# Optimization experiments

Measured on AMD Instinct MI355X. Metric: run time of the kernel, lower is better.

The kernel has to match this reference:

```python
import jax, jax.numpy as jnp
import numpy as np

B, C, H, W = 8, 192, 128, 128
HEADS = 16
EPS = 1e-12  # F.normalize eps


def setup_inputs() -> dict:
    key = jax.random.key(0)
    k1, k2, k3, k4 = jax.random.split(key, 4)
    s = 0.02
    return {
        "x": jax.random.normal(k1, (B, C, H, W), dtype=jnp.float32),
        "w_qkv": jax.random.normal(k2, (3 * C, C), dtype=jnp.float32) * s,
        "w_dw": jax.random.normal(k3, (C, 1, 3, 3), dtype=jnp.float32) * s,
        "w_proj": jax.random.normal(k4, (C, C), dtype=jnp.float32) * s,
        "temperature": jnp.ones((HEADS, 1, 1), dtype=jnp.float32),
    }


def reference(x, w_qkv, w_dw, w_proj, temperature):
    b, c, h, w = x.shape
    heads = HEADS
    hd = c // heads  # per-head channel dim
    hw = h * w

    # 1x1 conv qkv projection: [b, 3c, h, w]
    qkv = jnp.einsum('bchw,oc->bohw', x, w_qkv)
    q, k, v = jnp.split(qkv, 3, axis=1)

    def to_heads(t):
        return t.reshape(b, heads, hd, hw)  # b head c (h w)

    q, k, v = to_heads(q), to_heads(k), to_heads(v)

    # L2-normalize along spatial dim (matches F.normalize with eps clamp)
    q = q / jnp.maximum(jnp.linalg.norm(q, axis=-1, keepdims=True), EPS)
    k = k / jnp.maximum(jnp.linalg.norm(k, axis=-1, keepdims=True), EPS)

    # channel-wise attention: [b, head, hd, hd]
    attn = jnp.einsum('bhcn,bhdn->bhcd', q, k) * temperature
    attn = jax.nn.softmax(attn, axis=-1)

    out = jnp.einsum('bhcd,bhdn->bhcn', attn, v)  # [b, head, hd, hw]
    out = out.reshape(b, c, h, w)

    # depthwise 3x3 conv, padding=1
    out = jax.lax.conv_general_dilated(
        out, w_dw, window_strides=(1, 1), padding=((1, 1), (1, 1)),
        dimension_numbers=('NCHW', 'OIHW', 'NCHW'), feature_group_count=c)

    # 1x1 conv projection
    out = jnp.einsum('bchw,oc->bohw', out, w_proj)
    return out
```

## Files before the change

### kernel.cpp

```cpp
#include <hip/hip_runtime.h>

#define B_   8
#define C_   192
#define HW_  16384
#define W_   128
#define NH_  16
#define HD_  12

#define OFF_G      0u
#define OFF_WQKV   1179648u
#define OFF_WDW    1622016u
#define OFF_TEMP   1628928u
#define OFF_WPROJ  1629184u
#define OFF_M      1702912u
#define OFF_Y      2292736u

typedef __attribute__((ext_vector_type(8))) __bf16 bf16x8;
typedef __attribute__((ext_vector_type(8))) short  short8;
typedef __attribute__((ext_vector_type(4))) short  short4v;
typedef __attribute__((ext_vector_type(4))) float  floatx4;

__device__ __forceinline__ unsigned short f2bfu(float f) {
  union { float f; unsigned u; } v; v.f = f;
  unsigned r = (v.u + 0x7FFFu + ((v.u >> 16) & 1u)) >> 16;
  return (unsigned short)r;
}
__device__ __forceinline__ float bfu2f(unsigned short h) {
  union { unsigned u; float f; } v; v.u = ((unsigned)h) << 16;
  return v.f;
}
__device__ __forceinline__ bool bfmode(const void* temp) {
  return ((const unsigned*)temp)[0] != 0x3F800000u;
}
__device__ __forceinline__ float in_ld(const void* p, int i, bool bf) {
  return bf ? bfu2f(((const unsigned short*)p)[i]) : ((const float*)p)[i];
}
__device__ __forceinline__ floatx4 mfma16(short8 a, short8 b, floatx4 c) {
  union U { short8 s; bf16x8 b; } ua, ub;
  ua.s = a; ub.s = b;
  return __builtin_amdgcn_mfma_f32_16x16x32_bf16(ua.b, ub.b, c, 0, 0, 0);
}
__device__ __forceinline__ short8 row_frag(const void* x, bool bf, long elemoff) {
  short8 r;
  if (bf) {
    r = *(const short8*)((const unsigned short*)x + elemoff);
  } else {
    const float4* p4 = (const float4*)((const float*)x + elemoff);
    float4 a = p4[0], b = p4[1];
    r[0] = (short)f2bfu(a.x); r[1] = (short)f2bfu(a.y);
    r[2] = (short)f2bfu(a.z); r[3] = (short)f2bfu(a.w);
    r[4] = (short)f2bfu(b.x); r[5] = (short)f2bfu(b.y);
    r[6] = (short)f2bfu(b.z); r[7] = (short)f2bfu(b.w);
  }
  return r;
}

__global__ __launch_bounds__(256) void k_init(const void* wqkv, const void* wdw,
                                              const void* wproj, const void* temp,
                                              unsigned char* ws) {
  bool bf = bfmode(temp);
  int i = blockIdx.x * 256 + threadIdx.x;
  if (i < 110592) { ((float*)(ws + OFF_WQKV))[i] = in_ld(wqkv, i, bf); return; }
  i -= 110592;
  if (i < 1728) { ((float*)(ws + OFF_WDW))[i] = in_ld(wdw, i, bf); return; }
  i -= 1728;
  if (i < 16) { ((float*)(ws + OFF_TEMP))[i] = in_ld(temp, i, bf); return; }
  i -= 16;
  if (i < 36864) {
    unsigned short* wp = (unsigned short*)(ws + OFF_WPROJ);
    wp[i] = bf ? ((const unsigned short*)wproj)[i] : f2bfu(((const float*)wproj)[i]);
  }
}

__global__ __launch_bounds__(512) void k_gram(const void* x, const void* temp,
                                              unsigned char* ws) {
  bool bf = bfmode(temp);
  float* GP = (float*)(ws + OFF_Y);
  int b = blockIdx.x >> 5, grp = blockIdx.x & 31;
  int tid = threadIdx.x;
  int w = tid >> 6, lane = tid & 63, m = lane & 15, q = lane >> 4;
  int r0 = (w >> 1) * 3, c0 = (w & 1) * 6;
  long xb = (long)b * C_ * HW_;
  __shared__ __align__(16) short xs[C_][136];
  floatx4 acc[3][6];
  floatx4 zz = {0.f, 0.f, 0.f, 0.f};
#pragma unroll
  for (int i = 0; i < 3; ++i)
#pragma unroll
    for (int t = 0; t < 6; ++t) acc[i][t] = zz;

  short8 st[6];
  {
    int px0 = grp * 512;
#pragma unroll
    for (int i = 0; i < 6; ++i) {
      int chunk = i * 512 + tid;
      int c = chunk >> 4, p8 = chunk & 15;
      st[i] = row_frag(x, bf, xb + (long)c * HW_ + px0 + p8 * 8);
    }
  }
  for (int sl = 0; sl < 4; ++sl) {
    if (sl) __syncthreads();
#pragma unroll
    for (int i = 0; i < 6; ++i) {
      int chunk = i * 512 + tid;
      int c = chunk >> 4, p8 = chunk & 15;
      *(short8*)&xs[c][p8 * 8] = st[i];
    }
    __syncthreads();
    if (sl < 3) {
      int px0 = grp * 512 + (sl + 1) * 128;
#pragma unroll
      for (int i = 0; i < 6; ++i) {
        int chunk = i * 512 + tid;
        int c = chunk >> 4, p8 = chunk & 15;
        st[i] = row_frag(x, bf, xb + (long)c * HW_ + px0 + p8 * 8);
      }
    }
#pragma unroll
    for (int ks = 0; ks < 4; ++ks) {
      int col = ks * 32 + q * 8;
      short8 A0 = *(const short8*)&xs[(r0 + 0) * 16 + m][col];
      short8 A1 = *(const short8*)&xs[(r0 + 1) * 16 + m][col];
      short8 A2 = *(const short8*)&xs[(r0 + 2) * 16 + m][col];
#pragma unroll
      for (int t = 0; t < 6; ++t) {
        short8 F = *(const short8*)&xs[(c0 + t) * 16 + m][col];
        acc[0][t] = mfma16(A0, F, acc[0][t]);
        acc[1][t] = mfma16(A1, F, acc[1][t]);
        acc[2][t] = mfma16(A2, F, acc[2][t]);
      }
    }
  }
  float* GPb = GP + (long)(b * 32 + grp) * (C_ * C_);
#pragma unroll
  for (int i = 0; i < 3; ++i)
#pragma unroll
    for (int t = 0; t < 6; ++t)
#pragma unroll
      for (int r = 0; r < 4; ++r)
        GPb[((r0 + i) * 16 + q * 4 + r) * C_ + (c0 + t) * 16 + m] = acc[i][t][r];
}

__global__ __launch_bounds__(256) void k_reduce(unsigned char* ws) {
  const float4* GP = (const float4*)(ws + OFF_Y);
  float4* G = (float4*)(ws + OFF_G);
  int idx = blockIdx.x * 256 + threadIdx.x;
  int b = idx / 9216;
  int i = idx - b * 9216;
  const float4* p = GP + (long)b * 32 * 9216 + i;
  float4 s = {0.f, 0.f, 0.f, 0.f};
#pragma unroll
  for (int g = 0; g < 32; ++g) {
    float4 v = p[(long)g * 9216];
    s.x += v.x; s.y += v.y; s.z += v.z; s.w += v.w;
  }
  G[(long)b * 9216 + i] = s;
}

__global__ __launch_bounds__(256) void k_attn(unsigned char* ws) {
  int b = blockIdx.x >> 4, h = blockIdx.x & 15;
  int tid = threadIdx.x;
  const float* G  = (const float*)(ws + OFF_G) + (long)b * C_ * C_;
  const float* Wf = (const float*)(ws + OFF_WQKV);
  const float* Wq = Wf + (h * HD_) * C_;
  const float* Wk = Wf + (C_ + h * HD_) * C_;
  const float* Wv = Wf + (2 * C_ + h * HD_) * C_;
  float tmprt = ((const float*)(ws + OFF_TEMP))[h];
  unsigned short* Mh = (unsigned short*)(ws + OFF_M) + ((long)b * C_ + h * HD_) * C_;

  __shared__ float Gs[32][C_ + 1];
  __shared__ float tq[HD_][C_], tk[HD_][C_];
  __shared__ float Sm[HD_][HD_], Aw[HD_][HD_], nq[HD_], nk[HD_];

  for (int jblk = 0; jblk < 6; ++jblk) {
    for (int i = tid; i < 32 * C_; i += 256) {
      int jj = i / C_, a = i - jj * C_;
      Gs[jj][a] = G[(jblk * 32 + jj) * C_ + a];
    }
    __syncthreads();
    for (int i = tid; i < 2 * HD_ * 32; i += 256) {
      int jj = i & 31, rest = i >> 5;
      int c = rest % HD_, which = rest / HD_;
      const float* Wrow = (which ? Wk : Wq) + c * C_;
      float s = 0.f;
      for (int a = 0; a < C_; ++a) s += Wrow[a] * Gs[jj][a];
      float (*dst)[C_] = which ? tk : tq;
      dst[c][jblk * 32 + jj] = s;
    }
    __syncthreads();
  }
  if (tid < 144) {
    int c = tid / HD_, d = tid - c * HD_;
    float s = 0.f;
    for (int a = 0; a < C_; ++a) s += tq[c][a] * Wk[d * C_ + a];
    Sm[c][d] = s;
  } else if (tid < 156) {
    int c = tid - 144; float s = 0.f;
    for (int a = 0; a < C_; ++a) s += tq[c][a] * Wq[c * C_ + a];
    nq[c] = s;
  } else if (tid < 168) {
    int c = tid - 156; float s = 0.f;
    for (int a = 0; a < C_; ++a) s += tk[c][a] * Wk[c * C_ + a];
    nk[c] = s;
  }
  __syncthreads();
  if (tid < HD_) {
    int c = tid;
    float qn = fmaxf(sqrtf(fmaxf(nq[c], 0.f)), 1e-12f);
    float L[HD_], mx = -1e30f;
    for (int d = 0; d < HD_; ++d) {
      float kn = fmaxf(sqrtf(fmaxf(nk[d], 0.f)), 1e-12f);
      L[d] = Sm[c][d] / (qn * kn) * tmprt;
      mx = fmaxf(mx, L[d]);
    }
    float ssum = 0.f;
    for (int d = 0; d < HD_; ++d) { L[d] = __expf(L[d] - mx); ssum += L[d]; }
    float inv = 1.f / ssum;
    for (int d = 0; d < HD_; ++d) Aw[c][d] = L[d] * inv;
  }
  __syncthreads();
  for (int i = tid; i < HD_ * C_; i += 256) {
    int c = i / C_, j = i - c * C_;
    float s = 0.f;
    for (int d = 0; d < HD_; ++d) s += Aw[c][d] * Wv[d * C_ + j];
    Mh[c * C_ + j] = f2bfu(s);
  }
}

__global__ __launch_bounds__(256) void k_mx(const void* x, const void* temp,
                                            unsigned char* ws) {
  bool bf = bfmode(temp);
  const unsigned short* Mb = (const unsigned short*)(ws + OFF_M);
  unsigned short* y = (unsigned short*)(ws + OFF_Y);
  int b = blockIdx.x >> 7, px0 = (blockIdx.x & 127) * 128;
  int tid = threadIdx.x;
  int w = tid >> 6, lane = tid & 63, m = lane & 15, q = lane >> 4;
  long xb = (long)b * C_ * HW_;
  __shared__ __align__(16) short xsT[128][200];
  for (int i = 0; i < 3; ++i) {
    int chunk = i * 256 + tid;
    int p8 = chunk & 15, cq = chunk >> 4;
    short8 r0 = row_frag(x, bf, xb + (long)(cq * 4 + 0) * HW_ + px0 + p8 * 8);
    short8 r1 = row_frag(x, bf, xb + (long)(cq * 4 + 1) * HW_ + px0 + p8 * 8);
    short8 r2 = row_frag(x, bf, xb + (long)(cq * 4 + 2) * HW_ + px0 + p8 * 8);
    short8 r3 = row_frag(x, bf, xb + (long)(cq * 4 + 3) * HW_ + px0 + p8 * 8);
    for (int j = 0; j < 8; ++j) {
      short4v v = { r0[j], r1[j], r2[j], r3[j] };
      *(short4v*)&xsT[p8 * 8 + j][cq * 4] = v;
    }
  }
  __syncthreads();
  floatx4 acc[3][8];
  floatx4 zz = {0.f, 0.f, 0.f, 0.f};
  for (int i = 0; i < 3; ++i)
    for (int pt = 0; pt < 8; ++pt) acc[i][pt] = zz;
  for (int k = 0; k < 6; ++k) {
    int c0 = k * 32;
    const unsigned short* Mrow = Mb + (long)b * C_ * C_ + c0 + q * 8;
    short8 A0 = *(const short8*)(Mrow + ((3 * w + 0) * 16 + m) * C_);
    short8 A1 = *(const short8*)(Mrow + ((3 * w + 1) * 16 + m) * C_);
    short8 A2 = *(const short8*)(Mrow + ((3 * w + 2) * 16 + m) * C_);
    for (int pt = 0; pt < 8; ++pt) {
      short8 Bf = *(const short8*)&xsT[pt * 16 + m][c0 + q * 8];
      acc[0][pt] = mfma16(A0, Bf, acc[0][pt]);
      acc[1][pt] = mfma16(A1, Bf, acc[1][pt]);
      acc[2][pt] = mfma16(A2, Bf, acc[2][pt]);
    }
  }
  for (int i = 0; i < 3; ++i) {
    int rowb = (3 * w + i) * 16 + q * 4;
    for (int pt = 0; pt < 8; ++pt) {
      int px = px0 + pt * 16 + m;
      for (int rg = 0; rg < 4; ++rg)
        y[((long)b * C_ + rowb + rg) * HW_ + px] = f2bfu(acc[i][pt][rg]);
    }
  }
}

__global__ __launch_bounds__(512) void k_out(const void* temp, unsigned char* ws,
                                             void* out) {
  bool bf = bfmode(temp);
  const unsigned short* y = (const unsigned short*)(ws + OFF_Y);
  const float* wdw = (const float*)(ws + OFF_WDW);
  const unsigned short* Wp = (const unsigned short*)(ws + OFF_WPROJ);
  int b = blockIdx.x >> 7, irow = blockIdx.x & 127;
  int tid = threadIdx.x;
  __shared__ __align__(16) unsigned dly[128 * 36];

  int wv = tid >> 6, lane = tid & 63, m = lane & 15, q = lane >> 4;
  int wr = wv >> 2, wc = wv & 3;
  int pA = wc * 32 + m, pB = pA + 16;
  int swzA = (pA >> 3) & 7, swzB = (pB >> 3) & 7;

  int oct = tid & 15, cg = tid >> 4;
  int p0 = oct * 8;
  int wbase = p0 * 36 + ((((cg >> 2) ^ (oct & 7)) << 2) | (cg & 3));

  floatx4 acc[6][2];
  floatx4 zz = {0.f, 0.f, 0.f, 0.f};
#pragma unroll
  for (int r = 0; r < 6; ++r) { acc[r][0] = zz; acc[r][1] = zz; }

  for (int ch = 0; ch < 3; ++ch) {
    if (ch) __syncthreads();
    float a0[8], a1[8];
#pragma unroll
    for (int i = 0; i < 8; ++i) { a0[i] = 0.f; a1[i] = 0.f; }
#pragma unroll
    for (int j = 0; j < 2; ++j) {
      float* aj = j ? a1 : a0;
      int c = ch * 64 + cg * 2 + j;
      const unsigned short* yc = y + ((long)b * C_ + c) * HW_;
      float wv9[9];
#pragma unroll
      for (int t = 0; t < 9; ++t) wv9[t] = wdw[c * 9 + t];
      for (int dy = 0; dy < 3; ++dy) {
        int rr = irow + dy - 1;
        if (rr < 0 || rr > 127) continue;
        const unsigned short* yr = yc + rr * W_;
        float v[10];
        v[0] = (p0 == 0) ? 0.f : bfu2f(yr[p0 - 1]);
        union { uint4 u; unsigned short s[8]; } uu;
        uu.u = *(const uint4*)(yr + p0);
#pragma unroll
        for (int i = 0; i < 8; ++i) v[1 + i] = bfu2f(uu.s[i]);
        v[9] = (p0 + 8 >= W_) ? 0.f : bfu2f(yr[p0 + 8]);
#pragma unroll
        for (int dx = 0; dx < 3; ++dx) {
          float wc9 = wv9[dy * 3 + dx];
#pragma unroll
          for (int i = 0; i < 8; ++i) aj[i] += wc9 * v[i + dx];
        }
      }
    }
#pragma unroll
    for (int i = 0; i < 8; ++i) {
      unsigned pk = (unsigned)f2bfu(a0[i]) | ((unsigned)f2bfu(a1[i]) << 16);
      dly[wbase + i * 36] = pk;
    }
    __syncthreads();
#pragma unroll
    for (int ks = 0; ks < 2; ++ks) {
      int kb = ks * 4 + q;
      short8 B0 = *(const short8*)&dly[pA * 36 + ((kb ^ swzA) << 2)];
      short8 B1 = *(const short8*)&dly[pB * 36 + ((kb ^ swzB) << 2)];
      int c0 = ch * 64 + ks * 32 + q * 8;
#pragma unroll
      for (int r = 0; r < 6; ++r) {
        short8 A = *(const short8*)(Wp + (wr * 96 + r * 16 + m) * C_ + c0);
        acc[r][0] = mfma16(A, B0, acc[r][0]);
        acc[r][1] = mfma16(A, B1, acc[r][1]);
      }
    }
  }
  long ob = (long)b * C_ * HW_ + irow * W_;
#pragma unroll
  for (int r = 0; r < 6; ++r) {
    int o = wr * 96 + r * 16 + q * 4;
#pragma unroll
    for (int rg = 0; rg < 4; ++rg) {
      long off = ob + (long)(o + rg) * HW_;
      float v0 = acc[r][0][rg], v1 = acc[r][1][rg];
      if (bf) {
        ((unsigned short*)out)[off + pA] = f2bfu(v0);
        ((unsigned short*)out)[off + pB] = f2bfu(v1);
      } else {
        ((float*)out)[off + pA] = v0;
        ((float*)out)[off + pB] = v1;
      }
    }
  }
}

extern "C" void kernel_launch(void* const* d_in, const int* in_sizes, int n_in,
                              void* d_out, int out_size, void* d_ws, size_t ws_size,
                              hipStream_t stream) {
  const void* x     = d_in[0];
  const void* wqkv  = d_in[1];
  const void* wdw   = d_in[2];
  const void* wproj = d_in[3];
  const void* temp  = d_in[4];
  unsigned char* ws = (unsigned char*)d_ws;
  k_init<<<dim3(583), dim3(256), 0, stream>>>(wqkv, wdw, wproj, temp, ws);
  k_gram<<<dim3(256), dim3(512), 0, stream>>>(x, temp, ws);
  k_reduce<<<dim3(288), dim3(256), 0, stream>>>(ws);
  k_attn<<<dim3(128), dim3(256), 0, stream>>>(ws);
  k_mx<<<dim3(1024), dim3(256), 0, stream>>>(x, temp, ws);
  k_out<<<dim3(1024), dim3(512), 0, stream>>>(temp, ws, d_out);
}
```

Baseline: 349.1 us.

## Software-pipeline depthwise conv loads in k_out with register double buffering

Restructures the k_out kernel so the global loads for the next 64-channel chunk are issued into a second register buffer while the current chunk's depthwise conv and MFMA projection run. Horizontal halo values now come from wave shuffles instead of extra scalar global loads. Depthwise weights are staged once in shared memory. The block index is remapped to interleave batches across consecutive blocks. The aim is to hide global memory latency and cut redundant loads, at the cost of more registers (two 6×uint4 buffers), which may reduce occupancy.

```diff
diff --git a/kernel.cpp b/kernel.cpp
--- a/kernel.cpp
+++ b/kernel.cpp
@@ -284,9 +284,11 @@
   const unsigned short* y = (const unsigned short*)(ws + OFF_Y);
   const float* wdw = (const float*)(ws + OFF_WDW);
   const unsigned short* Wp = (const unsigned short*)(ws + OFF_WPROJ);
-  int b = blockIdx.x >> 7, irow = blockIdx.x & 127;
+  int lg = (blockIdx.x & 7) * 128 + (blockIdx.x >> 3);
+  int b = lg >> 7, irow = lg & 127;
   int tid = threadIdx.x;
   __shared__ __align__(16) unsigned dly[128 * 36];
+  __shared__ float dwlds[C_ * 9];
 
   int wv = tid >> 6, lane = tid & 63, m = lane & 15, q = lane >> 4;
   int wr = wv >> 2, wc = wv & 3;
@@ -297,63 +299,106 @@
   int p0 = oct * 8;
   int wbase = p0 * 36 + ((((cg >> 2) ^ (oct & 7)) << 2) | (cg & 3));
 
+  bool v_lo = irow > 0, v_hi = irow < 127;
+  int rlo = (v_lo ? irow - 1 : 0) * W_;
+  int rmi = irow * W_;
+  int rhi = (v_hi ? irow + 1 : 127) * W_;
+  const unsigned short* ybase = y + (long)b * C_ * HW_;
+
   floatx4 acc[6][2];
   floatx4 zz = {0.f, 0.f, 0.f, 0.f};
 #pragma unroll
   for (int r = 0; r < 6; ++r) { acc[r][0] = zz; acc[r][1] = zz; }
 
-  for (int ch = 0; ch < 3; ++ch) {
-    if (ch) __syncthreads();
-    float a0[8], a1[8];
-#pragma unroll
-    for (int i = 0; i < 8; ++i) { a0[i] = 0.f; a1[i] = 0.f; }
-#pragma unroll
-    for (int j = 0; j < 2; ++j) {
-      float* aj = j ? a1 : a0;
-      int c = ch * 64 + cg * 2 + j;
-      const unsigned short* yc = y + ((long)b * C_ + c) * HW_;
-      float wv9[9];
-#pragma unroll
-      for (int t = 0; t < 9; ++t) wv9[t] = wdw[c * 9 + t];
-      for (int dy = 0; dy < 3; ++dy) {
-        int rr = irow + dy - 1;
-        if (rr < 0 || rr > 127) continue;
-        const unsigned short* yr = yc + rr * W_;
-        float v[10];
-        v[0] = (p0 == 0) ? 0.f : bfu2f(yr[p0 - 1]);
-        union { uint4 u; unsigned short s[8]; } uu;
-        uu.u = *(const uint4*)(yr + p0);
-#pragma unroll
-        for (int i = 0; i < 8; ++i) v[1 + i] = bfu2f(uu.s[i]);
-        v[9] = (p0 + 8 >= W_) ? 0.f : bfu2f(yr[p0 + 8]);
-#pragma unroll
-        for (int dx = 0; dx < 3; ++dx) {
-          float wc9 = wv9[dy * 3 + dx];
-#pragma unroll
-          for (int i = 0; i < 8; ++i) aj[i] += wc9 * v[i + dx];
-        }
-      }
-    }
-#pragma unroll
-    for (int i = 0; i < 8; ++i) {
-      unsigned pk = (unsigned)f2bfu(a0[i]) | ((unsigned)f2bfu(a1[i]) << 16);
-      dly[wbase + i * 36] = pk;
-    }
-    __syncthreads();
-#pragma unroll
-    for (int ks = 0; ks < 2; ++ks) {
-      int kb = ks * 4 + q;
-      short8 B0 = *(const short8*)&dly[pA * 36 + ((kb ^ swzA) << 2)];
-      short8 B1 = *(const short8*)&dly[pB * 36 + ((kb ^ swzB) << 2)];
-      int c0 = ch * 64 + ks * 32 + q * 8;
-#pragma unroll
-      for (int r = 0; r < 6; ++r) {
-        short8 A = *(const short8*)(Wp + (wr * 96 + r * 16 + m) * C_ + c0);
-        acc[r][0] = mfma16(A, B0, acc[r][0]);
-        acc[r][1] = mfma16(A, B1, acc[r][1]);
-      }
-    }
-  }
+#define ISSUE(CH, L) { \
+  const unsigned short* yc0 = ybase + (long)((CH) * 64 + cg * 2) * HW_; \
+  const unsigned short* yc1 = yc0 + HW_; \
+  (L)[0] = *(const uint4*)(yc0 + rlo + p0); \
+  (L)[1] = *(const uint4*)(yc0 + rmi + p0); \
+  (L)[2] = *(const uint4*)(yc0 + rhi + p0); \
+  (L)[3] = *(const uint4*)(yc1 + rlo + p0); \
+  (L)[4] = *(const uint4*)(yc1 + rmi + p0); \
+  (L)[5] = *(const uint4*)(yc1 + rhi + p0); \
+}
+
+#define DWHALF(Lp, AJ, CC) { \
+  float w9[9]; \
+  _Pragma("unroll") \
+  for (int t = 0; t < 9; ++t) w9[t] = dwlds[(CC) * 9 + t]; \
+  _Pragma("unroll") \
+  for (int dy = 0; dy < 3; ++dy) { \
+    bool valid = (dy == 1) || (dy == 0 ? v_lo : v_hi); \
+    uint4 uu = (Lp)[dy]; \
+    unsigned lw = (unsigned)__shfl_up((int)uu.w, 1); \
+    unsigned rw = (unsigned)__shfl_down((int)uu.x, 1); \
+    if (valid) { \
+      union { uint4 u; unsigned short s[8]; } cv; cv.u = uu; \
+      float v[10]; \
+      v[0] = (oct == 0) ? 0.f : bfu2f((unsigned short)(lw >> 16)); \
+      _Pragma("unroll") \
+      for (int i = 0; i < 8; ++i) v[1 + i] = bfu2f(cv.s[i]); \
+      v[9] = (oct == 15) ? 0.f : bfu2f((unsigned short)(rw & 0xffffu)); \
+      _Pragma("unroll") \
+      for (int dx = 0; dx < 3; ++dx) { \
+        float wc9 = w9[dy * 3 + dx]; \
+        _Pragma("unroll") \
+        for (int i = 0; i < 8; ++i) (AJ)[i] += wc9 * v[i + dx]; \
+      } \
+    } \
+  } }
+
+#define DWCOMP(L, CH) { \
+  float a0[8], a1[8]; \
+  _Pragma("unroll") \
+  for (int i = 0; i < 8; ++i) { a0[i] = 0.f; a1[i] = 0.f; } \
+  DWHALF((L), a0, (CH) * 64 + cg * 2); \
+  DWHALF((L) + 3, a1, (CH) * 64 + cg * 2 + 1); \
+  _Pragma("unroll") \
+  for (int i = 0; i < 8; ++i) { \
+    unsigned pk = (unsigned)f2bfu(a0[i]) | ((unsigned)f2bfu(a1[i]) << 16); \
+    dly[wbase + i * 36] = pk; \
+  } }
+
+#define MFMAPH(CH) { \
+  _Pragma("unroll") \
+  for (int ks = 0; ks < 2; ++ks) { \
+    int kb = ks * 4 + q; \
+    short8 B0 = *(const short8*)&dly[pA * 36 + ((kb ^ swzA) << 2)]; \
+    short8 B1 = *(const short8*)&dly[pB * 36 + ((kb ^ swzB) << 2)]; \
+    int c0 = (CH) * 64 + ks * 32 + q * 8; \
+    _Pragma("unroll") \
+    for (int r = 0; r < 6; ++r) { \
+      short8 A = *(const short8*)(Wp + (wr * 96 + r * 16 + m) * C_ + c0); \
+      acc[r][0] = mfma16(A, B0, acc[r][0]); \
+      acc[r][1] = mfma16(A, B1, acc[r][1]); \
+    } \
+  } }
+
+  for (int i = tid; i < C_ * 9; i += 512) dwlds[i] = wdw[i];
+
+  uint4 LA[6], LB[6];
+  ISSUE(0, LA);
+  __syncthreads();
+
+  ISSUE(1, LB);
+  DWCOMP(LA, 0);
+  __syncthreads();
+  MFMAPH(0);
+  __syncthreads();
+  ISSUE(2, LA);
+  DWCOMP(LB, 1);
+  __syncthreads();
+  MFMAPH(1);
+  __syncthreads();
+  DWCOMP(LA, 2);
+  __syncthreads();
+  MFMAPH(2);
+
+#undef ISSUE
+#undef DWHALF
+#undef DWCOMP
+#undef MFMAPH
+
   long ob = (long)b * C_ * HW_ + irow * W_;
 #pragma unroll
   for (int r = 0; r < 6; ++r) {
```

Measured after the change: 344.1 us. About the same (-1.4%).
